# Optimization experiments

Measured on AMD Instinct MI355X. Metric: run time of the kernel, lower is better.

Reference implementation:

```python
import jax, jax.numpy as jnp
import numpy as np

E = 131072
IN_F = 64
OUT_F = 64
BOND_TYPE = 10  # num_type=4 -> 4*5/2
INIT_VAL = 0.01


def setup_inputs() -> dict:
    key = jax.random.key(0)
    k1, k2, k3, k4 = jax.random.split(key, 4)
    batch_ij = jax.random.randint(k1, (E,), 0, BOND_TYPE)
    batch_descriptor = jax.random.normal(k2, (E, IN_F, 1), dtype=jnp.float32)
    layer1 = INIT_VAL * jax.random.normal(k3, (BOND_TYPE, OUT_F, IN_F), dtype=jnp.float32)
    lin_w = INIT_VAL * jax.random.normal(k4, (OUT_F, IN_F), dtype=jnp.float32)
    lin_b = jnp.zeros((OUT_F,), dtype=jnp.float32)
    return {
        "batch_ij": batch_ij,
        "batch_descriptor": batch_descriptor,
        "layer1": layer1,
        "lin_w": lin_w,
        "lin_b": lin_b,
    }


def reference(batch_ij, batch_descriptor, layer1, lin_w, lin_b):
    # gather per-edge weight matrix by bond type, then batched matmul
    desc = batch_descriptor[..., 0]                       # [E, in]
    W_e = layer1[batch_ij]                                # [E, out, in] (large gather)
    out = jnp.einsum("eoi,ei->eo", W_e, desc)            # bmm
    out = jnp.tanh(out)                                   # ACT
    adjust = desc @ lin_w.T + lin_b                        # linear_adjust
    return (out + adjust)[..., None]                       # [E, out, 1]
```

## Files before the change

kernel.cpp:

```cpp
#include <hip/hip_runtime.h>
#include <hip/hip_bf16.h>

typedef __attribute__((ext_vector_type(8))) short bf16x8;
typedef __attribute__((ext_vector_type(4))) float f32x4;

#define NBLK 256

__device__ __forceinline__ unsigned short f2bf(float f) {
    unsigned u = __float_as_uint(f);
    return (unsigned short)((u + 0x7fffu + ((u >> 16) & 1u)) >> 16);
}

__device__ __forceinline__ bf16x8 pack8(float4 x, float4 y) {
    bf16x8 r;
    r[0] = (short)f2bf(x.x); r[1] = (short)f2bf(x.y);
    r[2] = (short)f2bf(x.z); r[3] = (short)f2bf(x.w);
    r[4] = (short)f2bf(y.x); r[5] = (short)f2bf(y.y);
    r[6] = (short)f2bf(y.z); r[7] = (short)f2bf(y.w);
    return r;
}

__device__ __forceinline__ float ftanh(float x) {
    float e = __expf(2.f * x);
    return 1.f - 2.f / (e + 1.f);
}

__global__ __launch_bounds__(1024, 4) void k_fused(
    const int* __restrict__ ij, const float* __restrict__ desc,
    const float* __restrict__ layer1, const float* __restrict__ lin_w,
    const float* __restrict__ lin_b, float* __restrict__ out, int E) {

    __shared__ __align__(16) short wsm[11 * 512 * 8];

    for (int idx = threadIdx.x; idx < 11 * 512; idx += 1024) {
        const int m = idx >> 9;
        const int fl = idx & 511;
        const int fi = fl >> 6, l = fl & 63;
        const int nt = fi >> 1, kk = fi & 1;
        const float* src = (m < 10) ? (layer1 + m * 4096) : lin_w;
        const float* sp = src + (nt * 16 + (l & 15)) * 64 + kk * 32 + (l >> 4) * 8;
        float4 x = *(const float4*)sp;
        float4 y = *(const float4*)(sp + 4);
        *(bf16x8*)(&wsm[idx * 8]) = pack8(x, y);
    }

    const int lane = threadIdx.x & 63;
    const int col = lane & 15;
    const int g = lane >> 4;
    const int kb = g * 8;
    const bf16x8 zero8 = {0, 0, 0, 0, 0, 0, 0, 0};

    __syncthreads();

    const int gw = blockIdx.x * 16 + (threadIdx.x >> 6);
    const int nst = (E + 31) >> 5;
    for (int s = gw; s < nst; s += NBLK * 16) {
        const int jb = s * 32;
        int e[2], ty[2];
        float4 d0[2], d1[2], d2[2], d3[2];
        #pragma unroll
        for (int p = 0; p < 2; ++p) {
            e[p] = jb + p * 16 + col;
            const int ec = min(e[p], E - 1);
            ty[p] = ij[ec];
            const float* dp = desc + (size_t)ec * 64 + kb;
            d0[p] = *(const float4*)dp;
            d1[p] = *(const float4*)(dp + 4);
            d2[p] = *(const float4*)(dp + 32);
            d3[p] = *(const float4*)(dp + 36);
        }
        bf16x8 b0[2], b1[2];
        #pragma unroll
        for (int p = 0; p < 2; ++p) {
            b0[p] = pack8(d0[p], d1[p]);
            b1[p] = pack8(d2[p], d3[p]);
        }

        #pragma unroll 1
        for (int nt = 0; nt < 4; ++nt) {
            f32x4 zL[2], zW[2];
            {
                const bf16x8 f0 = *(const bf16x8*)(&wsm[((80 + nt * 2 + 0) * 64 + lane) * 8]);
                const bf16x8 f1 = *(const bf16x8*)(&wsm[((80 + nt * 2 + 1) * 64 + lane) * 8]);
                #pragma unroll
                for (int p = 0; p < 2; ++p) {
                    f32x4 z = {0.f, 0.f, 0.f, 0.f};
                    z = __builtin_amdgcn_mfma_f32_16x16x32_bf16(f0, b0[p], z, 0, 0, 0);
                    zL[p] = __builtin_amdgcn_mfma_f32_16x16x32_bf16(f1, b1[p], z, 0, 0, 0);
                    zW[p] = (f32x4){0.f, 0.f, 0.f, 0.f};
                }
            }

            #pragma unroll 1
            for (int m = 0; m < 10; ++m) {
                const bf16x8 f0 = *(const bf16x8*)(&wsm[((m * 8 + nt * 2 + 0) * 64 + lane) * 8]);
                const bf16x8 f1 = *(const bf16x8*)(&wsm[((m * 8 + nt * 2 + 1) * 64 + lane) * 8]);
                #pragma unroll
                for (int p = 0; p < 2; ++p) {
                    const bf16x8 m0 = (ty[p] == m) ? b0[p] : zero8;
                    const bf16x8 m1 = (ty[p] == m) ? b1[p] : zero8;
                    zW[p] = __builtin_amdgcn_mfma_f32_16x16x32_bf16(f0, m0, zW[p], 0, 0, 0);
                    zW[p] = __builtin_amdgcn_mfma_f32_16x16x32_bf16(f1, m1, zW[p], 0, 0, 0);
                }
            }

            const float4 bias = *(const float4*)(lin_b + nt * 16 + g * 4);
            #pragma unroll
            for (int p = 0; p < 2; ++p) {
                if (e[p] < E) {
                    f32x4 r;
                    r[0] = ftanh(zW[p][0]) + zL[p][0] + bias.x;
                    r[1] = ftanh(zW[p][1]) + zL[p][1] + bias.y;
                    r[2] = ftanh(zW[p][2]) + zL[p][2] + bias.z;
                    r[3] = ftanh(zW[p][3]) + zL[p][3] + bias.w;
                    *(f32x4*)(out + (size_t)e[p] * 64 + nt * 16 + g * 4) = r;
                }
            }
        }
    }
}

extern "C" void kernel_launch(void* const* d_in, const int* in_sizes, int n_in,
                              void* d_out, int out_size, void* d_ws, size_t ws_size,
                              hipStream_t stream) {
    const int* ij = (const int*)d_in[0];
    const float* desc = (const float*)d_in[1];
    const float* layer1 = (const float*)d_in[2];
    const float* lin_w = (const float*)d_in[3];
    const float* lin_b = (const float*)d_in[4];
    float* out = (float*)d_out;
    const int E = in_sizes[0];

    k_fused<<<NBLK, 1024, 0, stream>>>(ij, desc, layer1, lin_w, lin_b, out, E);
}
```

Baseline: 30.02 us.

## Process 16-edge tiles with type-outer loop and skip absent bond types

Each wave now handles one 16-edge tile instead of two, and the loop order becomes bond type outer, output tile inner. A wave-wide __any check skips the MFMA work for bond types that no edge in the tile uses. With 10 random types over 16 edges, few types are skipped, so the main gain would come from hoisting the masking out of the inner loop and from better instruction-level parallelism across four independent accumulators. The cost is more live accumulator registers and a divergence-free branch per type.

Measured after the change: 26.34 us. 1.14x faster.

```diff
diff --git a/kernel.cpp b/kernel.cpp
--- a/kernel.cpp
+++ b/kernel.cpp
@@ -53,68 +53,53 @@
     __syncthreads();
 
     const int gw = blockIdx.x * 16 + (threadIdx.x >> 6);
-    const int nst = (E + 31) >> 5;
-    for (int s = gw; s < nst; s += NBLK * 16) {
-        const int jb = s * 32;
-        int e[2], ty[2];
-        float4 d0[2], d1[2], d2[2], d3[2];
+    const int ntl = (E + 15) >> 4;
+    for (int s = gw; s < ntl; s += NBLK * 16) {
+        const int e = s * 16 + col;
+        const int ec = min(e, E - 1);
+        const int ty = ij[ec];
+        const float* dp = desc + (size_t)ec * 64 + kb;
+        const float4 x0 = *(const float4*)dp,        y0 = *(const float4*)(dp + 4);
+        const float4 x1 = *(const float4*)(dp + 32), y1 = *(const float4*)(dp + 36);
+        const bf16x8 b0 = pack8(x0, y0);
+        const bf16x8 b1 = pack8(x1, y1);
+
+        f32x4 zL[4], zW[4];
         #pragma unroll
-        for (int p = 0; p < 2; ++p) {
-            e[p] = jb + p * 16 + col;
-            const int ec = min(e[p], E - 1);
-            ty[p] = ij[ec];
-            const float* dp = desc + (size_t)ec * 64 + kb;
-            d0[p] = *(const float4*)dp;
-            d1[p] = *(const float4*)(dp + 4);
-            d2[p] = *(const float4*)(dp + 32);
-            d3[p] = *(const float4*)(dp + 36);
-        }
-        bf16x8 b0[2], b1[2];
-        #pragma unroll
-        for (int p = 0; p < 2; ++p) {
-            b0[p] = pack8(d0[p], d1[p]);
-            b1[p] = pack8(d2[p], d3[p]);
+        for (int nt = 0; nt < 4; ++nt) {
+            const bf16x8 f0 = *(const bf16x8*)(&wsm[((80 + nt * 2 + 0) * 64 + lane) * 8]);
+            const bf16x8 f1 = *(const bf16x8*)(&wsm[((80 + nt * 2 + 1) * 64 + lane) * 8]);
+            f32x4 z = {0.f, 0.f, 0.f, 0.f};
+            z = __builtin_amdgcn_mfma_f32_16x16x32_bf16(f0, b0, z, 0, 0, 0);
+            zL[nt] = __builtin_amdgcn_mfma_f32_16x16x32_bf16(f1, b1, z, 0, 0, 0);
+            zW[nt] = (f32x4){0.f, 0.f, 0.f, 0.f};
         }
 
         #pragma unroll 1
-        for (int nt = 0; nt < 4; ++nt) {
-            f32x4 zL[2], zW[2];
-            {
-                const bf16x8 f0 = *(const bf16x8*)(&wsm[((80 + nt * 2 + 0) * 64 + lane) * 8]);
-                const bf16x8 f1 = *(const bf16x8*)(&wsm[((80 + nt * 2 + 1) * 64 + lane) * 8]);
-                #pragma unroll
-                for (int p = 0; p < 2; ++p) {
-                    f32x4 z = {0.f, 0.f, 0.f, 0.f};
-                    z = __builtin_amdgcn_mfma_f32_16x16x32_bf16(f0, b0[p], z, 0, 0, 0);
-                    zL[p] = __builtin_amdgcn_mfma_f32_16x16x32_bf16(f1, b1[p], z, 0, 0, 0);
-                    zW[p] = (f32x4){0.f, 0.f, 0.f, 0.f};
-                }
-            }
-
-            #pragma unroll 1
-            for (int m = 0; m < 10; ++m) {
+        for (int m = 0; m < 10; ++m) {
+            if (!__any(ty == m)) continue;
+            const bf16x8 m0 = (ty == m) ? b0 : zero8;
+            const bf16x8 m1 = (ty == m) ? b1 : zero8;
+            #pragma unroll
+            for (int nt = 0; nt < 4; ++nt) {
                 const bf16x8 f0 = *(const bf16x8*)(&wsm[((m * 8 + nt * 2 + 0) * 64 + lane) * 8]);
                 const bf16x8 f1 = *(const bf16x8*)(&wsm[((m * 8 + nt * 2 + 1) * 64 + lane) * 8]);
-                #pragma unroll
-                for (int p = 0; p < 2; ++p) {
-                    const bf16x8 m0 = (ty[p] == m) ? b0[p] : zero8;
-                    const bf16x8 m1 = (ty[p] == m) ? b1[p] : zero8;
-                    zW[p] = __builtin_amdgcn_mfma_f32_16x16x32_bf16(f0, m0, zW[p], 0, 0, 0);
-                    zW[p] = __builtin_amdgcn_mfma_f32_16x16x32_bf16(f1, m1, zW[p], 0, 0, 0);
-                }
+                zW[nt] = __builtin_amdgcn_mfma_f32_16x16x32_bf16(f0, m0, zW[nt], 0, 0, 0);
+                zW[nt] = __builtin_amdgcn_mfma_f32_16x16x32_bf16(f1, m1, zW[nt], 0, 0, 0);
             }
+        }
 
-            const float4 bias = *(const float4*)(lin_b + nt * 16 + g * 4);
+        if (e < E) {
+            float* op = out + (size_t)e * 64 + g * 4;
             #pragma unroll
-            for (int p = 0; p < 2; ++p) {
-                if (e[p] < E) {
-                    f32x4 r;
-                    r[0] = ftanh(zW[p][0]) + zL[p][0] + bias.x;
-                    r[1] = ftanh(zW[p][1]) + zL[p][1] + bias.y;
-                    r[2] = ftanh(zW[p][2]) + zL[p][2] + bias.z;
-                    r[3] = ftanh(zW[p][3]) + zL[p][3] + bias.w;
-                    *(f32x4*)(out + (size_t)e[p] * 64 + nt * 16 + g * 4) = r;
-                }
+            for (int nt = 0; nt < 4; ++nt) {
+                const float4 bias = *(const float4*)(lin_b + nt * 16 + g * 4);
+                f32x4 r;
+                r[0] = ftanh(zW[nt][0]) + zL[nt][0] + bias.x;
+                r[1] = ftanh(zW[nt][1]) + zL[nt][1] + bias.y;
+                r[2] = ftanh(zW[nt][2]) + zL[nt][2] + bias.z;
+                r[3] = ftanh(zW[nt][3]) + zL[nt][3] + bias.w;
+                *(f32x4*)(op + nt * 16) = r;
             }
         }
     }
```
